# Performance work log

Measured on AMD Instinct MI355X. Metric: run time of the kernel, lower is better.

The kernel has to match this reference:

```python
import jax, jax.numpy as jnp
import numpy as np

B, S, D, H, F = 64, 512, 512, 512, 8
G = 4 * H // F  # 256, rows of left Kronecker factors


def setup_inputs() -> dict:
    key = jax.random.key(0)
    ks = jax.random.split(key, 24)

    def n(k, shape, s=0.05):
        return jax.random.normal(k, shape, jnp.float32) * s

    return {
        "x": jax.random.normal(ks[0], (B, S, D), jnp.float32),
        "h0": jnp.zeros((2, B, H), jnp.float32),
        "c0": jnp.zeros((2, B, H), jnp.float32),
        # layer 1 (input dim D)
        "W11": n(ks[1], (G, 1)), "W12": n(ks[2], (F, D)),
        "U11": n(ks[3], (G, 1)), "U12": n(ks[4], (F, H)),
        "dW11": n(ks[5], (G, 1)), "dW12": n(ks[6], (F, D)),
        "dU11": n(ks[7], (G, 1)), "dU12": n(ks[8], (F, H)),
        "b11": n(ks[9], (4 * H, 1)), "b12": n(ks[10], (4 * H, 1)),
        # layer 2 (input dim H; init_weights reshapes W22 to (F, H))
        "W21": n(ks[11], (G, 1)), "W22": n(ks[12], (F, H)),
        "U21": n(ks[13], (G, 1)), "U22": n(ks[14], (F, H)),
        "dW21": n(ks[15], (G, 1)), "dW22": n(ks[16], (F, H)),
        "dU21": n(ks[17], (G, 1)), "dU22": n(ks[18], (F, H)),
        "b21": n(ks[19], (4 * H, 1)), "b22": n(ks[20], (4 * H, 1)),
    }


def _kron_col(a, M):
    # kron of column vector a:(G,1) with M:(F,B) -> (G*F, B) = (4H, B)
    return (a[:, :, None] * M[None, :, :]).reshape(a.shape[0] * M.shape[0], M.shape[1])


def _cell(xt, ht, ct, p):
    # xt:(B,Din) ht,ct:(B,H); gates computed as (4H,B) like the torch code
    W1, W2, U1, U2, dW1, dW2, dU1, dU2, b1, b2 = p
    g = (_kron_col(W1, W2 @ xt.T) + _kron_col(dW1, dW2 @ xt.T)
         + _kron_col(U1, U2 @ ht.T) + _kron_col(dU1, dU2 @ ht.T)
         + b1 + b2)
    i = jax.nn.sigmoid(g[:H])
    f = jax.nn.sigmoid(g[H:2 * H])
    gg = jnp.tanh(g[2 * H:3 * H])
    o = jax.nn.sigmoid(g[3 * H:])
    c = f * ct.T + i * gg            # (H,B)
    h = o * jnp.tanh(c)              # (H,B)
    return h.T, c.T                  # (B,H)


def reference(x, h0, c0,
              W11, W12, U11, U12, dW11, dW12, dU11, dU12, b11, b12,
              W21, W22, U21, U22, dW21, dW22, dU21, dU22, b21, b22):
    layers = [
        (W11, W12, U11, U12, dW11, dW12, dU11, dU12, b11, b12),
        (W21, W22, U21, U22, dW21, dW22, dU21, dU22, b21, b22),
    ]

    def step(carry, xt):
        h, c = carry  # each (2,B,H)
        inp = xt
        hs, cs = [], []
        for li in range(2):
            hn, cn = _cell(inp, h[li], c[li], layers[li])
            hs.append(hn)
            cs.append(cn)
            inp = hn
        return (jnp.stack(hs), jnp.stack(cs)), inp

    (hn, cn), seq = jax.lax.scan(step, (h0, c0), jnp.swapaxes(x, 0, 1))
    hidden_seq = jnp.swapaxes(seq, 0, 1)  # (B,S,H)
    return hidden_seq, hn, cn
```

## Files before the change

### kernel.cpp

```cpp
#include <hip/hip_runtime.h>
#include <math.h>

#define NB 64
#define NS 512
#define ND 512
#define NH 512
#define L2E 1.4426950408889634f

__device__ __forceinline__ float dpp_sum64(float x) {
    x += __int_as_float(__builtin_amdgcn_update_dpp(0, __float_as_int(x), 0x111, 0xf, 0xf, true));
    x += __int_as_float(__builtin_amdgcn_update_dpp(0, __float_as_int(x), 0x112, 0xf, 0xf, true));
    x += __int_as_float(__builtin_amdgcn_update_dpp(0, __float_as_int(x), 0x114, 0xf, 0xf, true));
    x += __int_as_float(__builtin_amdgcn_update_dpp(0, __float_as_int(x), 0x118, 0xf, 0xf, true));
    x += __int_as_float(__builtin_amdgcn_update_dpp(0, __float_as_int(x), 0x142, 0xa, 0xf, true));
    x += __int_as_float(__builtin_amdgcn_update_dpp(0, __float_as_int(x), 0x143, 0xc, 0xf, true));
    return x;
}

__device__ __forceinline__ float bcast63(float x) {
    return __int_as_float(__builtin_amdgcn_readlane(__float_as_int(x), 63));
}
__device__ __forceinline__ float rcp_fast(float x) { return __builtin_amdgcn_rcpf(x); }
__device__ __forceinline__ float exp2_fast(float x) {
    float r;
    asm("v_exp_f32 %0, %1" : "=v"(r) : "v"(x));
    return r;
}
__device__ __forceinline__ void wg_barrier() {
    asm volatile("s_waitcnt lgkmcnt(0)\n\ts_barrier" ::: "memory");
}

__device__ __forceinline__ float dot8s(const float* s, float4 x0, float4 x1) {
    float r = s[0] * x0.x;
    r = fmaf(s[1], x0.y, r); r = fmaf(s[2], x0.z, r); r = fmaf(s[3], x0.w, r);
    r = fmaf(s[4], x1.x, r); r = fmaf(s[5], x1.y, r); r = fmaf(s[6], x1.z, r);
    r = fmaf(s[7], x1.w, r);
    return r;
}

#define LW(mat, f, arr)                                                       \
    {                                                                         \
        const float* M = (mat) + (f) * NH;                                    \
        arr[0] = M[kb];     arr[1] = M[kb + 8];                               \
        arr[2] = M[kb + 16]; arr[3] = M[kb + 24];                             \
        arr[4] = M[kb + 4]; arr[5] = M[kb + 12];                              \
        arr[6] = M[kb + 20]; arr[7] = M[kb + 28];                             \
    }

#define GATEX(t1, t2, m3, m4, bb, cS, hS)                                     \
    {                                                                         \
        float g0 = fmaf(cw[0], (t1), fmaf(cdw[0], (t2), fmaf(cu[0], (m3), fmaf(cdu[0], (m4), bb[0])))); \
        float g1 = fmaf(cw[1], (t1), fmaf(cdw[1], (t2), fmaf(cu[1], (m3), fmaf(cdu[1], (m4), bb[1])))); \
        float g2 = fmaf(cw[2], (t1), fmaf(cdw[2], (t2), fmaf(cu[2], (m3), fmaf(cdu[2], (m4), bb[2])))); \
        float g3 = fmaf(cw[3], (t1), fmaf(cdw[3], (t2), fmaf(cu[3], (m3), fmaf(cdu[3], (m4), bb[3])))); \
        float ig = rcp_fast(1.0f + exp2_fast(g0));                            \
        float fg = rcp_fast(1.0f + exp2_fast(g1));                            \
        float gg = fmaf(-2.0f, rcp_fast(1.0f + exp2_fast(g2)), 1.0f);         \
        float og = rcp_fast(1.0f + exp2_fast(g3));                            \
        cS = fmaf(fg, cS, ig * gg);                                           \
        hS = og * fmaf(-2.0f, rcp_fast(1.0f + exp2_fast(cS * (2.0f * L2E))), 1.0f); \
    }

__global__ __launch_bounds__(64) void precomp_kernel(
    const float* __restrict__ x, const float* __restrict__ W12,
    const float* __restrict__ dW12, float* __restrict__ PT) {
    int bt = blockIdx.x;
    int l = threadIdx.x;
    const float4* xr = (const float4*)(x + (size_t)bt * ND);
    float4 xv0 = xr[l];
    float4 xv1 = xr[64 + l];

    float acc[16];
#pragma unroll
    for (int f = 0; f < 8; ++f) {
        const float4* w = (const float4*)(W12 + f * ND);
        float4 a = w[l], b = w[64 + l];
        float s = a.x * xv0.x;
        s = fmaf(a.y, xv0.y, s); s = fmaf(a.z, xv0.z, s); s = fmaf(a.w, xv0.w, s);
        s = fmaf(b.x, xv1.x, s); s = fmaf(b.y, xv1.y, s); s = fmaf(b.z, xv1.z, s);
        s = fmaf(b.w, xv1.w, s);
        acc[f] = s;
        const float4* dw = (const float4*)(dW12 + f * ND);
        float4 c = dw[l], d = dw[64 + l];
        float u = c.x * xv0.x;
        u = fmaf(c.y, xv0.y, u); u = fmaf(c.z, xv0.z, u); u = fmaf(c.w, xv0.w, u);
        u = fmaf(d.x, xv1.x, u); u = fmaf(d.y, xv1.y, u); u = fmaf(d.z, xv1.z, u);
        u = fmaf(d.w, xv1.w, u);
        acc[8 + f] = u;
    }
#pragma unroll
    for (int f = 0; f < 16; ++f) acc[f] = dpp_sum64(acc[f]);

    if (l == 63) {
        float4* o = (float4*)(PT + (size_t)bt * 16);
#pragma unroll
        for (int g = 0; g < 4; ++g)
            o[g] = make_float4(acc[g], acc[g + 4], acc[8 + g], acc[12 + g]);
    }
}

__global__ __launch_bounds__(512, 2) void lstm_fused_kernel(
    const float* __restrict__ PT, const float* __restrict__ h0,
    const float* __restrict__ c0,
    const float* __restrict__ W11, const float* __restrict__ U11,
    const float* __restrict__ dW11, const float* __restrict__ dU11,
    const float* __restrict__ U12, const float* __restrict__ dU12,
    const float* __restrict__ b11, const float* __restrict__ b12,
    const float* __restrict__ W21, const float* __restrict__ U21,
    const float* __restrict__ dW21, const float* __restrict__ dU21,
    const float* __restrict__ W22, const float* __restrict__ dW22,
    const float* __restrict__ U22, const float* __restrict__ dU22,
    const float* __restrict__ b21, const float* __restrict__ b22,
    float* __restrict__ out) {
    int b = blockIdx.x;
    int tid = threadIdx.x;
    int wv = tid >> 6;
    int l = tid & 63;
    int g = wv & 3;
    int kb = 32 * (l & 15) + (l >> 4);
    int rA = 8 * l + g, rB = 8 * l + g + 4;

    __shared__ float Ps[NS * 16];
    __shared__ float hb1[2][NH];
    __shared__ float hb2[2][NH];
    __shared__ float mr[2][16];

    {
        const float4* src = (const float4*)(PT + (size_t)b * NS * 16);
        float4* dst = (float4*)Ps;
#pragma unroll
        for (int i = 0; i < 4; ++i) dst[tid + i * 512] = src[tid + i * 512];
    }

    float* hn = out + (size_t)NB * NS * NH;
    float* cn = hn + (size_t)2 * NB * NH;
    const float SQ[4] = {-L2E, -L2E, 2.0f * L2E, -L2E};

    if (wv < 4) {
        float wU0[8], wU1[8], wD0[8], wD1[8], wW0[8], wW1[8], wV0[8], wV1[8];
        LW(U12, g, wU0)      LW(U12, g + 4, wU1)
        LW(dU12, g, wD0)     LW(dU12, g + 4, wD1)
        LW(W22, g, wW0)      LW(W22, g + 4, wW1)
        LW(dW22, g, wV0)     LW(dW22, g + 4, wV1)

        float cw[4], cdw[4], cu[4], cdu[4], bbA[4], bbB[4];
#pragma unroll
        for (int q = 0; q < 4; ++q) {
            cw[q] = W11[q * 64 + l] * SQ[q];
            cdw[q] = dW11[q * 64 + l] * SQ[q];
            cu[q] = U11[q * 64 + l] * SQ[q];
            cdu[q] = dU11[q * 64 + l] * SQ[q];
            bbA[q] = (b11[q * NH + rA] + b12[q * NH + rA]) * SQ[q];
            bbB[q] = (b11[q * NH + rB] + b12[q * NH + rB]) * SQ[q];
        }
        float hA = h0[(size_t)b * NH + rA], hB = h0[(size_t)b * NH + rB];
        float cA = c0[(size_t)b * NH + rA], cB = c0[(size_t)b * NH + rB];
        hb1[0][64 * g + l] = hA;
        hb1[0][64 * (g + 4) + l] = hB;
        wg_barrier();

        for (int i = 0; i <= NS + 1; ++i) {
            if (i <= NS) {
                float4 x0 = *(const float4*)&hb1[i & 1][4 * l];
                float4 x1 = *(const float4*)&hb1[i & 1][256 + 4 * l];
                float rWa = dpp_sum64(dot8s(wW0, x0, x1));
                float rWb = dpp_sum64(dot8s(wW1, x0, x1));
                float rVa = dpp_sum64(dot8s(wV0, x0, x1));
                float rVb = dpp_sum64(dot8s(wV1, x0, x1));
                if (i > 0 && l == 63)
                    *(float4*)&mr[(i - 1) & 1][4 * g] =
                        make_float4(rWa, rWb, rVa, rVb);
                if (i < NS) {
                    float rUa = dpp_sum64(dot8s(wU0, x0, x1));
                    float rUb = dpp_sum64(dot8s(wU1, x0, x1));
                    float rDa = dpp_sum64(dot8s(wD0, x0, x1));
                    float rDb = dpp_sum64(dot8s(wD1, x0, x1));
                    float m3A = bcast63(rUa), m3B = bcast63(rUb);
                    float m4A = bcast63(rDa), m4B = bcast63(rDb);
                    float4 pv = *(const float4*)&Ps[i * 16 + 4 * g];
                    GATEX(pv.x, pv.z, m3A, m4A, bbA, cA, hA)
                    GATEX(pv.y, pv.w, m3B, m4B, bbB, cB, hB)
                    hb1[(i + 1) & 1][64 * g + l] = hA;
                    hb1[(i + 1) & 1][64 * (g + 4) + l] = hB;
                }
            }
            wg_barrier();
        }
        hn[(size_t)b * NH + rA] = hA;
        hn[(size_t)b * NH + rB] = hB;
        cn[(size_t)b * NH + rA] = cA;
        cn[(size_t)b * NH + rB] = cB;
    } else {
        float wU0[8], wU1[8], wD0[8], wD1[8];
        LW(U22, g, wU0)      LW(U22, g + 4, wU1)
        LW(dU22, g, wD0)     LW(dU22, g + 4, wD1)

        float cw[4], cdw[4], cu[4], cdu[4], bbA[4], bbB[4];
#pragma unroll
        for (int q = 0; q < 4; ++q) {
            cw[q] = W21[q * 64 + l] * SQ[q];
            cdw[q] = dW21[q * 64 + l] * SQ[q];
            cu[q] = U21[q * 64 + l] * SQ[q];
            cdu[q] = dU21[q * 64 + l] * SQ[q];
            bbA[q] = (b21[q * NH + rA] + b22[q * NH + rA]) * SQ[q];
            bbB[q] = (b21[q * NH + rB] + b22[q * NH + rB]) * SQ[q];
        }
        const float* h0p = h0 + (size_t)NB * NH + (size_t)b * NH;
        const float* c0p = c0 + (size_t)NB * NH + (size_t)b * NH;
        float hA = h0p[rA], hB = h0p[rB];
        float cA = c0p[rA], cB = c0p[rB];
        hb2[0][64 * g + l] = hA;
        hb2[0][64 * (g + 4) + l] = hB;
        wg_barrier();

        float* outb = out + (size_t)b * NS * NH;
        for (int i = 0; i <= NS + 1; ++i) {
            int s = i - 2;
            if (s >= 0) {
                float4 y0 = *(const float4*)&hb2[s & 1][4 * l];
                float4 y1 = *(const float4*)&hb2[s & 1][256 + 4 * l];
                float rUa = dpp_sum64(dot8s(wU0, y0, y1));
                float rUb = dpp_sum64(dot8s(wU1, y0, y1));
                float rDa = dpp_sum64(dot8s(wD0, y0, y1));
                float rDb = dpp_sum64(dot8s(wD1, y0, y1));
                float m5A = bcast63(rUa), m5B = bcast63(rUb);
                float m6A = bcast63(rDa), m6B = bcast63(rDb);
                float4 mv = *(const float4*)&mr[s & 1][4 * g];
                GATEX(mv.x, mv.z, m5A, m6A, bbA, cA, hA)
                GATEX(mv.y, mv.w, m5B, m6B, bbB, cB, hB)
                hb2[(s + 1) & 1][64 * g + l] = hA;
                hb2[(s + 1) & 1][64 * (g + 4) + l] = hB;
                outb[(size_t)s * NH + rA] = hA;
                outb[(size_t)s * NH + rB] = hB;
            }
            wg_barrier();
        }
        hn[(size_t)NB * NH + (size_t)b * NH + rA] = hA;
        hn[(size_t)NB * NH + (size_t)b * NH + rB] = hB;
        cn[(size_t)NB * NH + (size_t)b * NH + rA] = cA;
        cn[(size_t)NB * NH + (size_t)b * NH + rB] = cB;
    }
}

extern "C" void kernel_launch(void* const* d_in, const int* in_sizes, int n_in,
                              void* d_out, int out_size, void* d_ws, size_t ws_size,
                              hipStream_t stream) {
    const float* x = (const float*)d_in[0];
    const float* h0 = (const float*)d_in[1];
    const float* c0 = (const float*)d_in[2];
    const float* W11 = (const float*)d_in[3];
    const float* W12 = (const float*)d_in[4];
    const float* U11 = (const float*)d_in[5];
    const float* U12 = (const float*)d_in[6];
    const float* dW11 = (const float*)d_in[7];
    const float* dW12 = (const float*)d_in[8];
    const float* dU11 = (const float*)d_in[9];
    const float* dU12 = (const float*)d_in[10];
    const float* b11 = (const float*)d_in[11];
    const float* b12 = (const float*)d_in[12];
    const float* W21 = (const float*)d_in[13];
    const float* W22 = (const float*)d_in[14];
    const float* U21 = (const float*)d_in[15];
    const float* U22 = (const float*)d_in[16];
    const float* dW21 = (const float*)d_in[17];
    const float* dW22 = (const float*)d_in[18];
    const float* dU21 = (const float*)d_in[19];
    const float* dU22 = (const float*)d_in[20];
    const float* b21 = (const float*)d_in[21];
    const float* b22 = (const float*)d_in[22];

    float* PT = (float*)d_ws;
    float* out = (float*)d_out;

    hipLaunchKernelGGL(precomp_kernel, dim3(NB * NS), dim3(64), 0, stream,
                       x, W12, dW12, PT);
    hipLaunchKernelGGL(lstm_fused_kernel, dim3(NB), dim3(512), 0, stream,
                       PT, h0, c0,
                       W11, U11, dW11, dU11, U12, dU12, b11, b12,
                       W21, U21, dW21, dU21, W22, dW22, U22, dU22, b21, b22,
                       out);
}
```

Measured before the change: 414.0 us.

## Double wavefronts per LSTM block so each wave handles one row group

The fused LSTM kernel grows from 512 to 1024 threads, with 8 waves per layer instead of 4. Each wave now owns one Kronecker row group instead of two, which halves the serial dot products, DPP reductions and gate math per wave on each timestep. The precompute output is reordered into float2 pairs to match the new per-wave indexing. In exchange, each per-step barrier now synchronises 16 waves, and the 64 blocks still occupy only 64 CUs.

```diff
diff --git a/kernel.cpp b/kernel.cpp
--- a/kernel.cpp
+++ b/kernel.cpp
@@ -41,9 +41,9 @@
 #define LW(mat, f, arr)                                                       \
     {                                                                         \
         const float* M = (mat) + (f) * NH;                                    \
-        arr[0] = M[kb];     arr[1] = M[kb + 8];                               \
+        arr[0] = M[kb];      arr[1] = M[kb + 8];                              \
         arr[2] = M[kb + 16]; arr[3] = M[kb + 24];                             \
-        arr[4] = M[kb + 4]; arr[5] = M[kb + 12];                              \
+        arr[4] = M[kb + 4];  arr[5] = M[kb + 12];                             \
         arr[6] = M[kb + 20]; arr[7] = M[kb + 28];                             \
     }
 
@@ -92,14 +92,13 @@
     for (int f = 0; f < 16; ++f) acc[f] = dpp_sum64(acc[f]);
 
     if (l == 63) {
-        float4* o = (float4*)(PT + (size_t)bt * 16);
-#pragma unroll
-        for (int g = 0; g < 4; ++g)
-            o[g] = make_float4(acc[g], acc[g + 4], acc[8 + g], acc[12 + g]);
-    }
-}
-
-__global__ __launch_bounds__(512, 2) void lstm_fused_kernel(
+        float2* o = (float2*)(PT + (size_t)bt * 16);
+#pragma unroll
+        for (int g = 0; g < 8; ++g) o[g] = make_float2(acc[g], acc[8 + g]);
+    }
+}
+
+__global__ __launch_bounds__(1024, 4) void lstm_fused_kernel(
     const float* __restrict__ PT, const float* __restrict__ h0,
     const float* __restrict__ c0,
     const float* __restrict__ W11, const float* __restrict__ U11,
@@ -116,9 +115,9 @@
     int tid = threadIdx.x;
     int wv = tid >> 6;
     int l = tid & 63;
-    int g = wv & 3;
+    int g = wv & 7;
     int kb = 32 * (l & 15) + (l >> 4);
-    int rA = 8 * l + g, rB = 8 * l + g + 4;
+    int r = 8 * l + g;
 
     __shared__ float Ps[NS * 16];
     __shared__ float hb1[2][NH];
@@ -128,89 +127,73 @@
     {
         const float4* src = (const float4*)(PT + (size_t)b * NS * 16);
         float4* dst = (float4*)Ps;
-#pragma unroll
-        for (int i = 0; i < 4; ++i) dst[tid + i * 512] = src[tid + i * 512];
+        dst[tid] = src[tid];
+        dst[tid + 1024] = src[tid + 1024];
     }
 
     float* hn = out + (size_t)NB * NS * NH;
     float* cn = hn + (size_t)2 * NB * NH;
     const float SQ[4] = {-L2E, -L2E, 2.0f * L2E, -L2E};
 
-    if (wv < 4) {
-        float wU0[8], wU1[8], wD0[8], wD1[8], wW0[8], wW1[8], wV0[8], wV1[8];
-        LW(U12, g, wU0)      LW(U12, g + 4, wU1)
-        LW(dU12, g, wD0)     LW(dU12, g + 4, wD1)
-        LW(W22, g, wW0)      LW(W22, g + 4, wW1)
-        LW(dW22, g, wV0)     LW(dW22, g + 4, wV1)
-
-        float cw[4], cdw[4], cu[4], cdu[4], bbA[4], bbB[4];
+    if (wv < 8) {
+        float wU[8], wD[8], wW[8], wV[8];
+        LW(U12, g, wU)
+        LW(dU12, g, wD)
+        LW(W22, g, wW)
+        LW(dW22, g, wV)
+
+        float cw[4], cdw[4], cu[4], cdu[4], bb[4];
 #pragma unroll
         for (int q = 0; q < 4; ++q) {
             cw[q] = W11[q * 64 + l] * SQ[q];
             cdw[q] = dW11[q * 64 + l] * SQ[q];
             cu[q] = U11[q * 64 + l] * SQ[q];
             cdu[q] = dU11[q * 64 + l] * SQ[q];
-            bbA[q] = (b11[q * NH + rA] + b12[q * NH + rA]) * SQ[q];
-            bbB[q] = (b11[q * NH + rB] + b12[q * NH + rB]) * SQ[q];
-        }
-        float hA = h0[(size_t)b * NH + rA], hB = h0[(size_t)b * NH + rB];
-        float cA = c0[(size_t)b * NH + rA], cB = c0[(size_t)b * NH + rB];
+            bb[q] = (b11[q * NH + r] + b12[q * NH + r]) * SQ[q];
+        }
+        float hA = h0[(size_t)b * NH + r];
+        float cA = c0[(size_t)b * NH + r];
         hb1[0][64 * g + l] = hA;
-        hb1[0][64 * (g + 4) + l] = hB;
         wg_barrier();
 
         for (int i = 0; i <= NS + 1; ++i) {
             if (i <= NS) {
                 float4 x0 = *(const float4*)&hb1[i & 1][4 * l];
                 float4 x1 = *(const float4*)&hb1[i & 1][256 + 4 * l];
-                float rWa = dpp_sum64(dot8s(wW0, x0, x1));
-                float rWb = dpp_sum64(dot8s(wW1, x0, x1));
-                float rVa = dpp_sum64(dot8s(wV0, x0, x1));
-                float rVb = dpp_sum64(dot8s(wV1, x0, x1));
+                float rW = dpp_sum64(dot8s(wW, x0, x1));
+                float rV = dpp_sum64(dot8s(wV, x0, x1));
                 if (i > 0 && l == 63)
-                    *(float4*)&mr[(i - 1) & 1][4 * g] =
-                        make_float4(rWa, rWb, rVa, rVb);
+                    *(float2*)&mr[(i - 1) & 1][2 * g] = make_float2(rW, rV);
                 if (i < NS) {
-                    float rUa = dpp_sum64(dot8s(wU0, x0, x1));
-                    float rUb = dpp_sum64(dot8s(wU1, x0, x1));
-                    float rDa = dpp_sum64(dot8s(wD0, x0, x1));
-                    float rDb = dpp_sum64(dot8s(wD1, x0, x1));
-                    float m3A = bcast63(rUa), m3B = bcast63(rUb);
-                    float m4A = bcast63(rDa), m4B = bcast63(rDb);
-                    float4 pv = *(const float4*)&Ps[i * 16 + 4 * g];
-                    GATEX(pv.x, pv.z, m3A, m4A, bbA, cA, hA)
-                    GATEX(pv.y, pv.w, m3B, m4B, bbB, cB, hB)
+                    float rU = dpp_sum64(dot8s(wU, x0, x1));
+                    float rD = dpp_sum64(dot8s(wD, x0, x1));
+                    float m3 = bcast63(rU), m4 = bcast63(rD);
+                    float2 pv = *(const float2*)&Ps[i * 16 + 2 * g];
+                    GATEX(pv.x, pv.y, m3, m4, bb, cA, hA)
                     hb1[(i + 1) & 1][64 * g + l] = hA;
-                    hb1[(i + 1) & 1][64 * (g + 4) + l] = hB;
                 }
             }
             wg_barrier();
         }
-        hn[(size_t)b * NH + rA] = hA;
-        hn[(size_t)b * NH + rB] = hB;
-        cn[(size_t)b * NH + rA] = cA;
-        cn[(size_t)b * NH + rB] = cB;
+        hn[(size_t)b * NH + r] = hA;
+        cn[(size_t)b * NH + r] = cA;
     } else {
-        float wU0[8], wU1[8], wD0[8], wD1[8];
-        LW(U22, g, wU0)      LW(U22, g + 4, wU1)
-        LW(dU22, g, wD0)     LW(dU22, g + 4, wD1)
-
-        float cw[4], cdw[4], cu[4], cdu[4], bbA[4], bbB[4];
+        float wU[8], wD[8];
+        LW(U22, g, wU)
+        LW(dU22, g, wD)
+
+        float cw[4], cdw[4], cu[4], cdu[4], bb[4];
 #pragma unroll
         for (int q = 0; q < 4; ++q) {
             cw[q] = W21[q * 64 + l] * SQ[q];
             cdw[q] = dW21[q * 64 + l] * SQ[q];
             cu[q] = U21[q * 64 + l] * SQ[q];
             cdu[q] = dU21[q * 64 + l] * SQ[q];
-            bbA[q] = (b21[q * NH + rA] + b22[q * NH + rA]) * SQ[q];
-            bbB[q] = (b21[q * NH + rB] + b22[q * NH + rB]) * SQ[q];
-        }
-        const float* h0p = h0 + (size_t)NB * NH + (size_t)b * NH;
-        const float* c0p = c0 + (size_t)NB * NH + (size_t)b * NH;
-        float hA = h0p[rA], hB = h0p[rB];
-        float cA = c0p[rA], cB = c0p[rB];
+            bb[q] = (b21[q * NH + r] + b22[q * NH + r]) * SQ[q];
+        }
+        float hA = h0[(size_t)NB * NH + (size_t)b * NH + r];
+        float cA = c0[(size_t)NB * NH + (size_t)b * NH + r];
         hb2[0][64 * g + l] = hA;
-        hb2[0][64 * (g + 4) + l] = hB;
         wg_barrier();
 
         float* outb = out + (size_t)b * NS * NH;
@@ -219,26 +202,18 @@
             if (s >= 0) {
                 float4 y0 = *(const float4*)&hb2[s & 1][4 * l];
                 float4 y1 = *(const float4*)&hb2[s & 1][256 + 4 * l];
-                float rUa = dpp_sum64(dot8s(wU0, y0, y1));
-                float rUb = dpp_sum64(dot8s(wU1, y0, y1));
-                float rDa = dpp_sum64(dot8s(wD0, y0, y1));
-                float rDb = dpp_sum64(dot8s(wD1, y0, y1));
-                float m5A = bcast63(rUa), m5B = bcast63(rUb);
-                float m6A = bcast63(rDa), m6B = bcast63(rDb);
-                float4 mv = *(const float4*)&mr[s & 1][4 * g];
-                GATEX(mv.x, mv.z, m5A, m6A, bbA, cA, hA)
-                GATEX(mv.y, mv.w, m5B, m6B, bbB, cB, hB)
+                float rU = dpp_sum64(dot8s(wU, y0, y1));
+                float rD = dpp_sum64(dot8s(wD, y0, y1));
+                float m5 = bcast63(rU), m6 = bcast63(rD);
+                float2 mv = *(const float2*)&mr[s & 1][2 * g];
+                GATEX(mv.x, mv.y, m5, m6, bb, cA, hA)
                 hb2[(s + 1) & 1][64 * g + l] = hA;
-                hb2[(s + 1) & 1][64 * (g + 4) + l] = hB;
-                outb[(size_t)s * NH + rA] = hA;
-                outb[(size_t)s * NH + rB] = hB;
+                outb[(size_t)s * NH + r] = hA;
             }
             wg_barrier();
         }
-        hn[(size_t)NB * NH + (size_t)b * NH + rA] = hA;
-        hn[(size_t)NB * NH + (size_t)b * NH + rB] = hB;
-        cn[(size_t)NB * NH + (size_t)b * NH + rA] = cA;
-        cn[(size_t)NB * NH + (size_t)b * NH + rB] = cB;
+        hn[(size_t)NB * NH + (size_t)b * NH + r] = hA;
+        cn[(size_t)NB * NH + (size_t)b * NH + r] = cA;
     }
 }
 
@@ -274,7 +249,7 @@
 
     hipLaunchKernelGGL(precomp_kernel, dim3(NB * NS), dim3(64), 0, stream,
                        x, W12, dW12, PT);
-    hipLaunchKernelGGL(lstm_fused_kernel, dim3(NB), dim3(512), 0, stream,
+    hipLaunchKernelGGL(lstm_fused_kernel, dim3(NB), dim3(1024), 0, stream,
                        PT, h0, c0,
                        W11, U11, dW11, dU11, U12, dU12, b11, b12,
                        W21, U21, dW21, dU21, W22, dW22, U22, dU22, b21, b22,
```

Result: slower. 430.8 us (+4.1%).
